# Kernel tuning notes

Measured on AMD Instinct MI355X. Metric: run time of the kernel, lower is better.

Reference implementation:

```python
import jax, jax.numpy as jnp
import numpy as np

H = 128          # hidden/context/decoder dim
HEADS = 4
HEAD_DIM = H // HEADS
MAX_LENGTH = 64
VOCAB = 3


def _lstm_step(h, c, x, Wih, Whh, b):
    # PyTorch gate order: i, f, g, o
    gates = x @ Wih.T + h @ Whh.T + b
    i, f, g, o = jnp.split(gates, 4, axis=-1)
    c = jax.nn.sigmoid(f) * c + jax.nn.sigmoid(i) * jnp.tanh(g)
    h = jax.nn.sigmoid(o) * jnp.tanh(c)
    return h, c


def _run_lstm(x, Wih, Whh, b):
    # x: (T, B, D) -> (T, B, H); zero initial state (PyTorch default)
    B = x.shape[1]
    Hh = Whh.shape[1]
    init = (jnp.zeros((B, Hh), x.dtype), jnp.zeros((B, Hh), x.dtype))
    def step(carry, xt):
        h, c = carry
        h, c = _lstm_step(h, c, xt, Wih, Whh, b)
        return (h, c), h
    _, ys = jax.lax.scan(step, init, x)
    return ys


def setup_inputs() -> dict:
    key = jax.random.key(0)
    T, B, D = 512, 64, 1024
    ks = jax.random.split(key, 20)
    def p(k, shape, s=0.05):
        return jax.random.normal(k, shape, dtype=jnp.float32) * s
    return {
        "cnn_output": p(ks[0], (T, B, D), 1.0),
        # encoder LSTM (2 layers); biases fused (b_ih + b_hh)
        "enc_Wih0": p(ks[1], (4 * H, D)),
        "enc_Whh0": p(ks[2], (4 * H, H)),
        "enc_b0": p(ks[3], (4 * H,)),
        "enc_Wih1": p(ks[4], (4 * H, H)),
        "enc_Whh1": p(ks[5], (4 * H, H)),
        "enc_b1": p(ks[6], (4 * H,)),
        # MultiheadAttention(embed_dim=128, num_heads=4)
        "attn_in_w": p(ks[7], (3 * H, H)),
        "attn_in_b": p(ks[8], (3 * H,)),
        "attn_out_w": p(ks[9], (H, H)),
        "attn_out_b": p(ks[10], (H,)),
        # decoder LSTM (2 layers), input dim 256
        "dec_Wih0": p(ks[11], (4 * H, 2 * H)),
        "dec_Whh0": p(ks[12], (4 * H, H)),
        "dec_b0": p(ks[13], (4 * H,)),
        "dec_Wih1": p(ks[14], (4 * H, H)),
        "dec_Whh1": p(ks[15], (4 * H, H)),
        "dec_b1": p(ks[16], (4 * H,)),
        # output projection
        "lin_w": p(ks[17], (VOCAB, H)),
        "lin_b": p(ks[18], (VOCAB,)),
    }


def reference(cnn_output, enc_Wih0, enc_Whh0, enc_b0, enc_Wih1, enc_Whh1, enc_b1,
              attn_in_w, attn_in_b, attn_out_w, attn_out_b,
              dec_Wih0, dec_Whh0, dec_b0, dec_Wih1, dec_Whh1, dec_b1,
              lin_w, lin_b):
    T, B, _ = cnn_output.shape
    # ---- encoder: 2-layer LSTM over T ----
    enc = _run_lstm(cnn_output, enc_Wih0, enc_Whh0, enc_b0)
    enc = _run_lstm(enc, enc_Wih1, enc_Whh1, enc_b1)          # (T, B, H)

    # ---- precompute attention keys/values (encoding is fixed) ----
    Wq, Wk, Wv = jnp.split(attn_in_w, 3, axis=0)
    bq, bk, bv = jnp.split(attn_in_b, 3, axis=0)
    K = (enc @ Wk.T + bk).reshape(T, B, HEADS, HEAD_DIM)      # (T,B,h,d)
    V = (enc @ Wv.T + bv).reshape(T, B, HEADS, HEAD_DIM)
    scale = 1.0 / np.sqrt(HEAD_DIM)

    # ---- 64-step attention + 2-layer LSTM decode loop ----
    out0 = jnp.zeros((B, H), cnn_output.dtype)
    h0 = jnp.zeros((2, B, H), cnn_output.dtype)
    c0 = jnp.zeros((2, B, H), cnn_output.dtype)

    def step(carry, _):
        out, h, c = carry
        q = ((out @ Wq.T + bq) * scale).reshape(B, HEADS, HEAD_DIM)
        scores = jnp.einsum("bhd,tbhd->bht", q, K)            # (B,h,T)
        attn = jax.nn.softmax(scores, axis=-1)
        ctx = jnp.einsum("bht,tbhd->bhd", attn, V).reshape(B, H)
        ctx = ctx @ attn_out_w.T + attn_out_b
        x = jnp.concatenate([out, ctx], axis=-1)              # (B, 2H)
        nh0, nc0 = _lstm_step(h[0], c[0], x, dec_Wih0, dec_Whh0, dec_b0)
        nh1, nc1 = _lstm_step(h[1], c[1], nh0, dec_Wih1, dec_Whh1, dec_b1)
        new_out = jax.nn.relu(nh1)
        y = new_out @ lin_w.T + lin_b                          # (B, vocab)
        return (new_out, jnp.stack([nh0, nh1]), jnp.stack([nc0, nc1])), y

    _, ys = jax.lax.scan(step, (out0, h0, c0), None, length=MAX_LENGTH)
    return ys                                                  # (64, B, vocab)
```

## Files before the change

### kernel.cpp

```cpp
#include <hip/hip_runtime.h>
#include <math.h>

#define T_LEN 512
#define BATCH 64
#define HID 128
#define G4 512

#define OFF_WQ2   0
#define OFF_WXO   16384
#define OFF_WXC   81920
#define OFF_WHH0b 147456
#define OFF_WIH1b 212992
#define OFF_WHH1b 278528
#define W2_TOTAL  344064

typedef __attribute__((ext_vector_type(8))) short short8b;
typedef __attribute__((ext_vector_type(4))) float f32x4;

__device__ __forceinline__ float sigf(float x) { return 1.0f / (1.0f + __expf(-x)); }
__device__ __forceinline__ float tanhfast(float x) {
    float e = __expf(2.f * x);
    return 1.f - 2.f / (e + 1.f);
}

__device__ __forceinline__ unsigned short f2bf(float x) {
    unsigned u = __float_as_uint(x);
    unsigned r = (u + 0x7fffu + ((u >> 16) & 1u)) >> 16;
    return (unsigned short)r;
}
__device__ __forceinline__ float bf2f(unsigned short u) {
    return __uint_as_float((unsigned)u << 16);
}

__device__ __forceinline__ void cvt8(uint4 u, float f[8]) {
    f[0] = __uint_as_float(u.x << 16); f[1] = __uint_as_float(u.x & 0xffff0000u);
    f[2] = __uint_as_float(u.y << 16); f[3] = __uint_as_float(u.y & 0xffff0000u);
    f[4] = __uint_as_float(u.z << 16); f[5] = __uint_as_float(u.z & 0xffff0000u);
    f[6] = __uint_as_float(u.w << 16); f[7] = __uint_as_float(u.w & 0xffff0000u);
}

#define KEEP4(Vv) asm volatile("" : "+v"((Vv).x), "+v"((Vv).y), "+v"((Vv).z), "+v"((Vv).w))

__device__ __forceinline__ void cstore(float* p, float v) {
    __hip_atomic_store(p, v, __ATOMIC_RELAXED, __HIP_MEMORY_SCOPE_AGENT);
}
__device__ __forceinline__ float cload(float* p) {
    return __hip_atomic_load(p, __ATOMIC_RELAXED, __HIP_MEMORY_SCOPE_AGENT);
}

__global__ __launch_bounds__(256) void pack_bf(
    const float* __restrict__ src, unsigned short* __restrict__ dst, long n8)
{
    long i = (long)blockIdx.x * 256 + threadIdx.x;
    long stride = (long)gridDim.x * 256;
    for (; i < n8; i += stride) {
        const float* s = src + i * 8;
        float4 a = *(const float4*)s;
        float4 b = *(const float4*)(s + 4);
        uint4 o;
        o.x = (unsigned)f2bf(a.x) | ((unsigned)f2bf(a.y) << 16);
        o.y = (unsigned)f2bf(a.z) | ((unsigned)f2bf(a.w) << 16);
        o.z = (unsigned)f2bf(b.x) | ((unsigned)f2bf(b.y) << 16);
        o.w = (unsigned)f2bf(b.z) | ((unsigned)f2bf(b.w) << 16);
        *(uint4*)(dst + i * 8) = o;
    }
}

__global__ __launch_bounds__(256) void gemm_mfma_bf16(
    const unsigned short* __restrict__ A, const unsigned short* __restrict__ B,
    const float* __restrict__ bias, unsigned short* __restrict__ C,
    int M, int N, int K)
{
    __shared__ __align__(16) unsigned char As[128 * 128];
    __shared__ __align__(16) unsigned char Bs[128 * 128];
    const int tid = threadIdx.x;
    const int lane = tid & 63, wave = tid >> 6;
    const int wr = wave >> 1, wc = wave & 1;
    const int m0 = blockIdx.y * 128, n0 = blockIdx.x * 128;
    f32x4 acc[4][4] = {};
    const int lr = lane & 15, g = lane >> 4;

    for (int k0 = 0; k0 < K; k0 += 64) {
        __syncthreads();
        #pragma unroll
        for (int i = 0; i < 4; ++i) {
            int c = tid + i * 256;
            int row = c >> 3, cb = (c & 7) * 16;
            int swz = cb ^ ((row & 7) << 4);
            uint4 va = *(const uint4*)(A + (size_t)(m0 + row) * K + k0 + (c & 7) * 8);
            *(uint4*)(As + row * 128 + swz) = va;
            uint4 vb = *(const uint4*)(B + (size_t)(n0 + row) * K + k0 + (c & 7) * 8);
            *(uint4*)(Bs + row * 128 + swz) = vb;
        }
        __syncthreads();
        #pragma unroll
        for (int kh = 0; kh < 2; ++kh) {
            const int cb = kh * 64 + g * 16;
            short8b af[4], bfr[4];
            #pragma unroll
            for (int m = 0; m < 4; ++m) {
                int row = wr * 64 + m * 16 + lr;
                af[m] = *(const short8b*)(As + row * 128 + (cb ^ ((row & 7) << 4)));
            }
            #pragma unroll
            for (int n = 0; n < 4; ++n) {
                int row = wc * 64 + n * 16 + lr;
                bfr[n] = *(const short8b*)(Bs + row * 128 + (cb ^ ((row & 7) << 4)));
            }
            #pragma unroll
            for (int m = 0; m < 4; ++m)
                #pragma unroll
                for (int n = 0; n < 4; ++n)
                    acc[m][n] = __builtin_amdgcn_mfma_f32_16x16x32_bf16(
                        af[m], bfr[n], acc[m][n], 0, 0, 0);
        }
    }
    #pragma unroll
    for (int n = 0; n < 4; ++n) {
        int col = n0 + wc * 64 + n * 16 + lr;
        float bv = bias[col];
        #pragma unroll
        for (int m = 0; m < 4; ++m) {
            #pragma unroll
            for (int j = 0; j < 4; ++j) {
                int row = m0 + wr * 64 + m * 16 + g * 4 + j;
                C[(size_t)row * N + col] = f2bf(acc[m][n][j] + bv);
            }
        }
    }
}

__global__ __launch_bounds__(1024) void lstm_rec3(
    const unsigned short* __restrict__ X,
    const float* __restrict__ Whh,
    unsigned short* __restrict__ HoutB)
{
    const int b = blockIdx.x;
    const int tid = threadIdx.x;
    const int r = tid >> 1, half = tid & 1;
    __shared__ __align__(16) float h_s[HID];
    __shared__ float gate_s[G4];
    float4 w4[16];
    {
        const float4* wr4 = (const float4*)(Whh + (size_t)r * HID + half * 64);
        #pragma unroll
        for (int i = 0; i < 16; ++i) w4[i] = wr4[i];
    }
    float c = 0.f;
    if (tid < HID) h_s[tid] = 0.f;
    __syncthreads();
    float xc0 = 0.f, xc1 = 0.f, xc2 = 0.f, xc3 = 0.f;
    if (half == 0) {
        xc0 = bf2f(X[(size_t)(0 * BATCH + b) * G4 + r]);
        xc1 = bf2f(X[(size_t)(1 * BATCH + b) * G4 + r]);
        xc2 = bf2f(X[(size_t)(2 * BATCH + b) * G4 + r]);
        xc3 = bf2f(X[(size_t)(3 * BATCH + b) * G4 + r]);
    }
    for (int tc = 0; tc < T_LEN; tc += 4) {
        float xn0 = 0.f, xn1 = 0.f, xn2 = 0.f, xn3 = 0.f;
        if (half == 0 && tc + 4 < T_LEN) {
            xn0 = bf2f(X[(size_t)((tc + 4) * BATCH + b) * G4 + r]);
            xn1 = bf2f(X[(size_t)((tc + 5) * BATCH + b) * G4 + r]);
            xn2 = bf2f(X[(size_t)((tc + 6) * BATCH + b) * G4 + r]);
            xn3 = bf2f(X[(size_t)((tc + 7) * BATCH + b) * G4 + r]);
        }
        #pragma unroll
        for (int i = 0; i < 4; ++i) {
            const int t = tc + i;
            const float xv = (i == 0) ? xc0 : (i == 1) ? xc1 : (i == 2) ? xc2 : xc3;
            float a0 = 0.f, a1 = 0.f, a2 = 0.f, a3 = 0.f;
            const float4* h4 = (const float4*)(h_s + half * 64);
            #pragma unroll
            for (int k = 0; k < 16; ++k) {
                float4 hv = h4[k];
                a0 = fmaf(w4[k].x, hv.x, a0);
                a1 = fmaf(w4[k].y, hv.y, a1);
                a2 = fmaf(w4[k].z, hv.z, a2);
                a3 = fmaf(w4[k].w, hv.w, a3);
            }
            float tot = (a0 + a1) + (a2 + a3);
            tot += __shfl_xor(tot, 1);
            if (half == 0) gate_s[r] = tot + xv;
            __syncthreads();
            if (tid < HID) {
                float gi = gate_s[tid], gf = gate_s[HID+tid], gg = gate_s[2*HID+tid], go = gate_s[3*HID+tid];
                c = sigf(gf) * c + sigf(gi) * tanhfast(gg);
                float h = sigf(go) * tanhfast(c);
                h_s[tid] = h;
                HoutB[(size_t)(t * BATCH + b) * HID + tid] = f2bf(h);
            }
            __syncthreads();
        }
        xc0 = xn0; xc1 = xn1; xc2 = xn2; xc3 = xn3;
    }
}

__global__ __launch_bounds__(256) void kv_pack_bf(
    const unsigned short* __restrict__ KVbf, unsigned short* __restrict__ Kb,
    unsigned short* __restrict__ Vt)
{
    const int b = blockIdx.x & 63, tc = blockIdx.x >> 6;
    const int t0 = tc * 128;
    __shared__ unsigned short tile[128][130];
    const int half = threadIdx.x >> 7;
    const int d = threadIdx.x & 127;
    for (int tt = 0; tt < 128; tt += 2) {
        int trow = tt + half;
        int t = t0 + trow;
        const unsigned short* src = KVbf + ((size_t)t * BATCH + b) * 256;
        Kb[((size_t)b * T_LEN + t) * HID + d] = src[d];
        tile[trow][d] = src[128 + d];
    }
    __syncthreads();
    for (int dd = 0; dd < 128; dd += 2) {
        int drow = dd + half;
        int ts = threadIdx.x & 127;
        Vt[((size_t)b * HID + drow) * T_LEN + t0 + ts] = tile[ts][drow];
    }
}

__global__ __launch_bounds__(256) void pack2(
    const float* __restrict__ attn_in_w,
    const float* __restrict__ dWih0, const float* __restrict__ dWhh0,
    const float* __restrict__ dWih1, const float* __restrict__ dWhh1,
    unsigned short* __restrict__ Wb2)
{
    int i = blockIdx.x * 256 + threadIdx.x;
    if (i >= W2_TOTAL) return;
    if (i >= OFF_WXC && i < OFF_WHH0b) return;
    float v;
    if (i < OFF_WXO) v = attn_in_w[i];
    else if (i < OFF_WXC) {
        int j = i - OFF_WXO; v = dWih0[(size_t)(j >> 7) * 256 + (j & 127)];
    }
    else if (i < OFF_WIH1b) v = dWhh0[i - OFF_WHH0b];
    else if (i < OFF_WHH1b) v = dWih1[i - OFF_WIH1b];
    else                    v = dWhh1[i - OFF_WHH1b];
    Wb2[i] = f2bf(v);
}

__global__ __launch_bounds__(256) void fuse_wxc(
    const float* __restrict__ dWih0, const float* __restrict__ ow,
    unsigned short* __restrict__ Wb2)
{
    __shared__ float ow_s[128 * 128];
    for (int i = threadIdx.x; i < 16384; i += 256) ow_s[i] = ow[i];
    __syncthreads();
    const int r = blockIdx.x * 2 + (threadIdx.x >> 7);
    const int c = threadIdx.x & 127;
    const float* wr = dWih0 + (size_t)r * 256 + 128;
    float acc = 0.f;
    #pragma unroll 8
    for (int j = 0; j < 128; ++j) acc = fmaf(wr[j], ow_s[j * 128 + c], acc);
    Wb2[OFF_WXC + r * 128 + c] = f2bf(acc);
}

__global__ __launch_bounds__(128) void fuse_b0(
    const float* __restrict__ dWih0, const float* __restrict__ ob,
    const float* __restrict__ db0, float* __restrict__ b0p)
{
    int r = blockIdx.x * 128 + threadIdx.x;
    const float* wr = dWih0 + (size_t)r * 256 + 128;
    float acc = db0[r];
    #pragma unroll 8
    for (int j = 0; j < 128; ++j) acc = fmaf(wr[j], ob[j], acc);
    b0p[r] = acc;
}

__global__ __launch_bounds__(512, 2) void decoder7c(
    const unsigned short* __restrict__ Kb, const unsigned short* __restrict__ Vt,
    const unsigned short* __restrict__ Wb2, const float* __restrict__ b0p,
    const float* __restrict__ attn_b, const float* __restrict__ b1,
    const float* __restrict__ lw, const float* __restrict__ lb,
    int* __restrict__ flags, float* __restrict__ exh0, float* __restrict__ exh1,
    float* __restrict__ Y)
{
    extern __shared__ __align__(16) char dyn[];
    char* Kl = dyn;
    const int wid = blockIdx.x;
    const int b = wid & 63;
    const int half64 = wid >> 6;
    const int dbase = half64 * 64;
    const int pbase = 64 - dbase;
    const int tid = threadIdx.x;
    int* myflag = flags + wid * 16;
    int* pflag  = flags + (wid ^ 64) * 16;
    float* exh0b = exh0 + b * 256;
    float* exh1b = exh1 + b * 256;

    __shared__ __align__(16) float x_s[384];
    __shared__ __align__(16) float x1_s[256];
    __shared__ __align__(16) float q_s[HID];
    __shared__ __align__(16) float sc[4 * T_LEN];
    __shared__ float red[512];
    __shared__ __align__(16) float ctxp[4][HID];
    __shared__ float g_s[256];
    __shared__ float hden[4];

    {
        const unsigned short* Ksrc = Kb + (size_t)b * T_LEN * HID;
        for (int c = tid; c < T_LEN * HID / 8; c += 512) {
            int t = c >> 4, k16 = c & 15;
            uint4 v = *(const uint4*)(Ksrc + c * 8);
            *(uint4*)(Kl + t * 256 + ((k16 * 16) ^ ((t & 15) << 4))) = v;
        }
    }
    const int lr = tid >> 1, halfk = tid & 1;
    const int r0 = (lr >> 6) * 128 + dbase + (lr & 63);
    uint4 W0[24], W1[16], WQ[4];
    #pragma unroll
    for (int i = 0; i < 24; ++i) {
        int ge = halfk * 192 + i * 8;
        const unsigned short* src =
            (ge < 128) ? Wb2 + OFF_WXO   + (size_t)r0 * HID + ge
          : (ge < 256) ? Wb2 + OFF_WXC   + (size_t)r0 * HID + (ge - 128)
                       : Wb2 + OFF_WHH0b + (size_t)r0 * HID + (ge - 256);
        W0[i] = *(const uint4*)src;
    }
    #pragma unroll
    for (int i = 0; i < 16; ++i) {
        int ge = halfk * 128 + i * 8;
        const unsigned short* src =
            (ge < 128) ? Wb2 + OFF_WIH1b + (size_t)r0 * HID + ge
                       : Wb2 + OFF_WHH1b + (size_t)r0 * HID + (ge - 128);
        W1[i] = *(const uint4*)src;
    }
    const int qrow = tid >> 2, qpart = tid & 3;
    #pragma unroll
    for (int i = 0; i < 4; ++i)
        WQ[i] = *(const uint4*)(Wb2 + OFF_WQ2 + (size_t)qrow * HID + qpart * 32 + i * 8);
    #pragma unroll
    for (int i = 0; i < 24; ++i) KEEP4(W0[i]);
    #pragma unroll
    for (int i = 0; i < 16; ++i) KEEP4(W1[i]);
    #pragma unroll
    for (int i = 0; i < 4; ++i) KEEP4(WQ[i]);

    const float b0r = b0p[r0];
    const float b1r = b1[r0];
    const float bqv = attn_b[qrow];
    float c0 = 0.f, c1 = 0.f;
    if (tid < 384) x_s[tid] = 0.f;
    if (tid < 256) x1_s[tid] = 0.f;
    __syncthreads();
    const float scale = 0.17677669529663687f;
    const int g = tid >> 7, l = tid & 127;

    for (int step = 0; step < 64; ++step) {
        #pragma unroll
        for (int i = 0; i < 24; ++i) KEEP4(W0[i]);
        #pragma unroll
        for (int i = 0; i < 16; ++i) KEEP4(W1[i]);
        #pragma unroll
        for (int i = 0; i < 4; ++i) KEEP4(WQ[i]);
        const int par = step & 1;
        if (step > 0) {
            if (tid == 0)
                while (__hip_atomic_load(pflag, __ATOMIC_RELAXED, __HIP_MEMORY_SCOPE_AGENT) < 2*step + 1)
                    __builtin_amdgcn_s_sleep(1);
            asm volatile("" ::: "memory");
            __syncthreads();
            if (tid < 64) {
                float hp = cload(&exh1b[((step - 1) & 1) * 128 + pbase + tid]);
                x1_s[128 + pbase + tid] = hp;
                x_s[pbase + tid] = fmaxf(hp, 0.f);
            }
            __syncthreads();
        }
        if (step > 0 && half64 == 0 && tid < 24) {
            const int row = tid >> 3, part = tid & 7;
            const float* wr = lw + row * HID + part * 16;
            const float* os = x_s + part * 16;
            float acc = 0.f;
            #pragma unroll
            for (int k = 0; k < 16; ++k) acc = fmaf(wr[k], os[k], acc);
            acc += __shfl_xor(acc, 1);
            acc += __shfl_xor(acc, 2);
            acc += __shfl_xor(acc, 4);
            if (part == 0) Y[((size_t)(step - 1) * BATCH + b) * 3 + row] = acc + lb[row];
        }
        {
            float acc = 0.f;
            const float* os = x_s + qpart * 32;
            #pragma unroll
            for (int i = 0; i < 4; ++i) {
                float f[8]; cvt8(WQ[i], f);
                const float* o8 = os + i * 8;
                acc += f[0]*o8[0]+f[1]*o8[1]+f[2]*o8[2]+f[3]*o8[3]
                     + f[4]*o8[4]+f[5]*o8[5]+f[6]*o8[6]+f[7]*o8[7];
            }
            acc += __shfl_xor(acc, 1);
            acc += __shfl_xor(acc, 2);
            if (qpart == 0) q_s[qrow] = (acc + bqv) * scale;
        }
        __syncthreads();
        {
            const int t = tid;
            float acc[4] = {0.f, 0.f, 0.f, 0.f};
            #pragma unroll
            for (int k16 = 0; k16 < 16; ++k16) {
                uint4 u = *(const uint4*)(Kl + t * 256 + ((k16 * 16) ^ ((t & 15) << 4)));
                float f[8]; cvt8(u, f);
                float4 q0 = *(const float4*)(q_s + k16 * 8);
                float4 q1 = *(const float4*)(q_s + k16 * 8 + 4);
                acc[k16 >> 2] += f[0]*q0.x + f[1]*q0.y + f[2]*q0.z + f[3]*q0.w
                               + f[4]*q1.x + f[5]*q1.y + f[6]*q1.z + f[7]*q1.w;
            }
            #pragma unroll
            for (int h = 0; h < 4; ++h) sc[h * T_LEN + t] = __expf(acc[h]);
        }
        __syncthreads();
        {
            float s4 = 0.f;
            #pragma unroll
            for (int i = 0; i < 4; ++i) s4 += sc[g * T_LEN + l + 128 * i];
            red[tid] = s4;
        }
        __syncthreads();
        if (l < 64) {
            float s2 = red[g*128 + l] + red[g*128 + l + 64];
            #pragma unroll
            for (int s = 32; s > 0; s >>= 1) s2 += __shfl_xor(s2, s, 64);
            if (l == 0) hden[g] = s2;
        }
        __syncthreads();
        {
            const int d = tid & 127, ch = tid >> 7;
            const unsigned short* vr = Vt + ((size_t)b * HID + d) * T_LEN + ch * 128;
            const float* scr = sc + (d >> 5) * T_LEN + ch * 128;
            float acc = 0.f;
            #pragma unroll
            for (int k = 0; k < 128; k += 8) {
                float f[8]; cvt8(*(const uint4*)(vr + k), f);
                #pragma unroll
                for (int j = 0; j < 8; ++j) acc = fmaf(f[j], scr[k + j], acc);
            }
            ctxp[ch][d] = acc;
        }
        __syncthreads();
        if (tid < HID)
            x_s[HID + tid] = (ctxp[0][tid] + ctxp[1][tid] + ctxp[2][tid] + ctxp[3][tid]) / hden[tid >> 5];
        __syncthreads();
        {
            float acc = 0.f;
            #pragma unroll
            for (int i = 0; i < 24; ++i) {
                float f[8]; cvt8(W0[i], f);
                const float* xp = x_s + halfk * 192 + i * 8;
                acc += f[0]*xp[0]+f[1]*xp[1]+f[2]*xp[2]+f[3]*xp[3]
                     + f[4]*xp[4]+f[5]*xp[5]+f[6]*xp[6]+f[7]*xp[7];
            }
            acc += __shfl_xor(acc, 1);
            if (halfk == 0) g_s[lr] = acc + b0r;
        }
        __syncthreads();
        if (tid < 64) {
            float gi = g_s[tid], gf = g_s[64+tid], gg = g_s[128+tid], go = g_s[192+tid];
            c0 = sigf(gf) * c0 + sigf(gi) * tanhf(gg);
            float h = sigf(go) * tanhf(c0);
            x_s[256 + dbase + tid] = h;
            x1_s[dbase + tid] = h;
            cstore(&exh0b[par * 128 + dbase + tid], h);
        }
        __syncthreads();
        if (tid == 0) {
            asm volatile("s_waitcnt vmcnt(0)" ::: "memory");
            __hip_atomic_store(myflag, 2*step + 2, __ATOMIC_RELEASE, __HIP_MEMORY_SCOPE_AGENT);
        }
        if (tid == 0)
            while (__hip_atomic_load(pflag, __ATOMIC_ACQUIRE, __HIP_MEMORY_SCOPE_AGENT) < 2*step + 2)
                __builtin_amdgcn_s_sleep(1);
        asm volatile("" ::: "memory");
        __syncthreads();
        if (tid < 64) {
            float hp = cload(&exh0b[par * 128 + pbase + tid]);
            x_s[256 + pbase + tid] = hp;
            x1_s[pbase + tid] = hp;
        }
        __syncthreads();
        {
            float acc = 0.f;
            #pragma unroll
            for (int i = 0; i < 16; ++i) {
                float f[8]; cvt8(W1[i], f);
                const float* xp = x1_s + halfk * 128 + i * 8;
                acc += f[0]*xp[0]+f[1]*xp[1]+f[2]*xp[2]+f[3]*xp[3]
                     + f[4]*xp[4]+f[5]*xp[5]+f[6]*xp[6]+f[7]*xp[7];
            }
            acc += __shfl_xor(acc, 1);
            if (halfk == 0) g_s[lr] = acc + b1r;
        }
        __syncthreads();
        if (tid < 64) {
            float gi = g_s[tid], gf = g_s[64+tid], gg = g_s[128+tid], go = g_s[192+tid];
            c1 = sigf(gf) * c1 + sigf(gi) * tanhf(gg);
            float h = sigf(go) * tanhf(c1);
            x1_s[128 + dbase + tid] = h;
            x_s[dbase + tid] = fmaxf(h, 0.f);
            cstore(&exh1b[par * 128 + dbase + tid], h);
        }
        __syncthreads();
        if (tid == 0) {
            asm volatile("s_waitcnt vmcnt(0)" ::: "memory");
            __hip_atomic_store(myflag, 2*step + 3, __ATOMIC_RELEASE, __HIP_MEMORY_SCOPE_AGENT);
        }
        __syncthreads();
    }
    if (tid == 0)
        while (__hip_atomic_load(pflag, __ATOMIC_ACQUIRE, __HIP_MEMORY_SCOPE_AGENT) < 129)
            __builtin_amdgcn_s_sleep(1);
    asm volatile("" ::: "memory");
    __syncthreads();
    if (tid < 64)
        x_s[pbase + tid] = fmaxf(cload(&exh1b[128 + pbase + tid]), 0.f);
    __syncthreads();
    if (half64 == 0 && tid < 24) {
        const int row = tid >> 3, part = tid & 7;
        const float* wr = lw + row * HID + part * 16;
        const float* os = x_s + part * 16;
        float acc = 0.f;
        #pragma unroll
        for (int k = 0; k < 16; ++k) acc = fmaf(wr[k], os[k], acc);
        acc += __shfl_xor(acc, 1);
        acc += __shfl_xor(acc, 2);
        acc += __shfl_xor(acc, 4);
        if (part == 0) Y[((size_t)63 * BATCH + b) * 3 + row] = acc + lb[row];
    }
}

extern "C" void kernel_launch(void* const* d_in, const int* in_sizes, int n_in,
                              void* d_out, int out_size, void* d_ws, size_t ws_size,
                              hipStream_t stream) {
    const float* cnn        = (const float*)d_in[0];
    const float* eWih0      = (const float*)d_in[1];
    const float* eWhh0      = (const float*)d_in[2];
    const float* eb0        = (const float*)d_in[3];
    const float* eWih1      = (const float*)d_in[4];
    const float* eWhh1      = (const float*)d_in[5];
    const float* eb1        = (const float*)d_in[6];
    const float* attn_in_w  = (const float*)d_in[7];
    const float* attn_in_b  = (const float*)d_in[8];
    const float* attn_out_w = (const float*)d_in[9];
    const float* attn_out_b = (const float*)d_in[10];
    const float* dWih0      = (const float*)d_in[11];
    const float* dWhh0      = (const float*)d_in[12];
    const float* db0        = (const float*)d_in[13];
    const float* dWih1      = (const float*)d_in[14];
    const float* dWhh1      = (const float*)d_in[15];
    const float* db1        = (const float*)d_in[16];
    const float* lin_w      = (const float*)d_in[17];
    const float* lin_b      = (const float*)d_in[18];
    float* Y  = (float*)d_out;

    const int M = T_LEN * BATCH;

    char* wsb = (char*)d_ws;
    unsigned short* Xbf   = (unsigned short*)(wsb);
    unsigned short* Hbf   = (unsigned short*)(wsb + ((size_t)32 << 20));
    unsigned short* wih0b = (unsigned short*)(wsb + ((size_t)40 << 20));
    unsigned short* wih1b = (unsigned short*)(wsb + ((size_t)41 << 20));
    unsigned short* wkvb  = (unsigned short*)(wsb + ((size_t)41 << 20) + (512 << 10));
    unsigned short* Wb2   = (unsigned short*)(wsb + ((size_t)42 << 20));
    float* b0p   = (float*)(wsb + ((size_t)43 << 20));
    int*   flags = (int*)((char*)b0p + 4096);
    float* exh0  = (float*)((char*)flags + 16384);
    float* exh1  = exh0 + 64 * 256;
    unsigned short* cnn_bf = (unsigned short*)(wsb + ((size_t)44 << 20));
    unsigned short* KVbf   = cnn_bf;
    unsigned short* Kb     = (unsigned short*)(wsb + ((size_t)60 << 20));
    unsigned short* Vt     = (unsigned short*)(wsb + ((size_t)68 << 20));

    (void)hipFuncSetAttribute((const void*)decoder7c,
                              hipFuncAttributeMaxDynamicSharedMemorySize, 131072);

    pack_bf<<<2048, 256, 0, stream>>>(cnn, cnn_bf, (long)M * 1024 / 8);
    pack_bf<<<256, 256, 0, stream>>>(eWih0, wih0b, (long)512 * 1024 / 8);
    pack_bf<<<32, 256, 0, stream>>>(eWih1, wih1b, (long)512 * 128 / 8);
    pack_bf<<<16, 256, 0, stream>>>(attn_in_w + 128 * 128, wkvb, (long)256 * 128 / 8);
    gemm_mfma_bf16<<<dim3(4, M/128), 256, 0, stream>>>(cnn_bf, wih0b, eb0, Xbf, M, 512, 1024);
    (void)hipMemsetAsync(flags, 0, 16384 + 2 * 64 * 256 * 4, stream);
    pack2<<<(W2_TOTAL + 255) / 256, 256, 0, stream>>>(attn_in_w, dWih0, dWhh0, dWih1, dWhh1, Wb2);
    fuse_wxc<<<256, 256, 0, stream>>>(dWih0, attn_out_w, Wb2);
    fuse_b0<<<4, 128, 0, stream>>>(dWih0, attn_out_b, db0, b0p);
    lstm_rec3<<<BATCH, 1024, 0, stream>>>(Xbf, eWhh0, Hbf);
    gemm_mfma_bf16<<<dim3(4, M/128), 256, 0, stream>>>(Hbf, wih1b, eb1, Xbf, M, 512, 128);
    lstm_rec3<<<BATCH, 1024, 0, stream>>>(Xbf, eWhh1, Hbf);
    gemm_mfma_bf16<<<dim3(2, M/128), 256, 0, stream>>>(Hbf, wkvb, attn_in_b + 128, KVbf, M, 256, 128);
    kv_pack_bf<<<256, 256, 0, stream>>>(KVbf, Kb, Vt);
    decoder7c<<<128, 512, 131072, stream>>>(Kb, Vt, Wb2, b0p,
                                            attn_in_b, db1, lin_w, lin_b,
                                            flags, exh0, exh1, Y);
}
```

Before: 2.419 ms.

## Fuse two encoder LSTM layers into one wavefront-pipelined kernel with flags

Replaces the two sequential encoder LSTM launches and the layer-1 input GEMM with one kernel of 128 blocks. Blocks 0-63 run layer 0 and publish each h_t to global memory with a release flag. Blocks 64-127 spin on that flag and compute layer 1 with the input projection done inline from bf16 weights held in registers. This lets the two recurrences overlap in time instead of running back to back. The cost is cross-block spin synchronisation, per-step global round trips, and a requirement that all 128 blocks be co-resident, otherwise the kernel deadlocks.

Result: slower. 3.592 ms (+48.5%).

```diff
diff --git a/kernel.cpp b/kernel.cpp
--- a/kernel.cpp
+++ b/kernel.cpp
@@ -130,57 +130,130 @@
     }
 }
 
-__global__ __launch_bounds__(1024) void lstm_rec3(
+__global__ __launch_bounds__(1024, 1) void lstm_fused(
     const unsigned short* __restrict__ X,
-    const float* __restrict__ Whh,
+    const float* __restrict__ Whh0,
+    const unsigned short* __restrict__ Wih1b,
+    const unsigned short* __restrict__ Whh1b,
+    const float* __restrict__ b1v,
+    float* __restrict__ h0x,
+    int* __restrict__ lflags,
     unsigned short* __restrict__ HoutB)
 {
-    const int b = blockIdx.x;
+    const int wid = blockIdx.x;
+    const int b = wid & 63;
     const int tid = threadIdx.x;
     const int r = tid >> 1, half = tid & 1;
+    int* flag = lflags + b * 16;
     __shared__ __align__(16) float h_s[HID];
+    __shared__ __align__(16) float x0_s[HID];
     __shared__ float gate_s[G4];
-    float4 w4[16];
-    {
-        const float4* wr4 = (const float4*)(Whh + (size_t)r * HID + half * 64);
-        #pragma unroll
-        for (int i = 0; i < 16; ++i) w4[i] = wr4[i];
-    }
-    float c = 0.f;
-    if (tid < HID) h_s[tid] = 0.f;
-    __syncthreads();
-    float xc0 = 0.f, xc1 = 0.f, xc2 = 0.f, xc3 = 0.f;
-    if (half == 0) {
-        xc0 = bf2f(X[(size_t)(0 * BATCH + b) * G4 + r]);
-        xc1 = bf2f(X[(size_t)(1 * BATCH + b) * G4 + r]);
-        xc2 = bf2f(X[(size_t)(2 * BATCH + b) * G4 + r]);
-        xc3 = bf2f(X[(size_t)(3 * BATCH + b) * G4 + r]);
-    }
-    for (int tc = 0; tc < T_LEN; tc += 4) {
-        float xn0 = 0.f, xn1 = 0.f, xn2 = 0.f, xn3 = 0.f;
-        if (half == 0 && tc + 4 < T_LEN) {
-            xn0 = bf2f(X[(size_t)((tc + 4) * BATCH + b) * G4 + r]);
-            xn1 = bf2f(X[(size_t)((tc + 5) * BATCH + b) * G4 + r]);
-            xn2 = bf2f(X[(size_t)((tc + 6) * BATCH + b) * G4 + r]);
-            xn3 = bf2f(X[(size_t)((tc + 7) * BATCH + b) * G4 + r]);
-        }
-        #pragma unroll
-        for (int i = 0; i < 4; ++i) {
-            const int t = tc + i;
-            const float xv = (i == 0) ? xc0 : (i == 1) ? xc1 : (i == 2) ? xc2 : xc3;
-            float a0 = 0.f, a1 = 0.f, a2 = 0.f, a3 = 0.f;
-            const float4* h4 = (const float4*)(h_s + half * 64);
-            #pragma unroll
-            for (int k = 0; k < 16; ++k) {
-                float4 hv = h4[k];
-                a0 = fmaf(w4[k].x, hv.x, a0);
-                a1 = fmaf(w4[k].y, hv.y, a1);
-                a2 = fmaf(w4[k].z, hv.z, a2);
-                a3 = fmaf(w4[k].w, hv.w, a3);
-            }
-            float tot = (a0 + a1) + (a2 + a3);
-            tot += __shfl_xor(tot, 1);
-            if (half == 0) gate_s[r] = tot + xv;
+
+    if (wid < 64) {
+        float4 w4[16];
+        {
+            const float4* wr4 = (const float4*)(Whh0 + (size_t)r * HID + half * 64);
+            #pragma unroll
+            for (int i = 0; i < 16; ++i) w4[i] = wr4[i];
+        }
+        float c = 0.f;
+        if (tid < HID) h_s[tid] = 0.f;
+        __syncthreads();
+        float xc0 = 0.f, xc1 = 0.f, xc2 = 0.f, xc3 = 0.f;
+        if (half == 0) {
+            xc0 = bf2f(X[(size_t)(0 * BATCH + b) * G4 + r]);
+            xc1 = bf2f(X[(size_t)(1 * BATCH + b) * G4 + r]);
+            xc2 = bf2f(X[(size_t)(2 * BATCH + b) * G4 + r]);
+            xc3 = bf2f(X[(size_t)(3 * BATCH + b) * G4 + r]);
+        }
+        for (int tc = 0; tc < T_LEN; tc += 4) {
+            float xn0 = 0.f, xn1 = 0.f, xn2 = 0.f, xn3 = 0.f;
+            if (half == 0 && tc + 4 < T_LEN) {
+                xn0 = bf2f(X[(size_t)((tc + 4) * BATCH + b) * G4 + r]);
+                xn1 = bf2f(X[(size_t)((tc + 5) * BATCH + b) * G4 + r]);
+                xn2 = bf2f(X[(size_t)((tc + 6) * BATCH + b) * G4 + r]);
+                xn3 = bf2f(X[(size_t)((tc + 7) * BATCH + b) * G4 + r]);
+            }
+            #pragma unroll
+            for (int i = 0; i < 4; ++i) {
+                const int t = tc + i;
+                const float xv = (i == 0) ? xc0 : (i == 1) ? xc1 : (i == 2) ? xc2 : xc3;
+                float a0 = 0.f, a1 = 0.f, a2 = 0.f, a3 = 0.f;
+                const float4* h4 = (const float4*)(h_s + half * 64);
+                #pragma unroll
+                for (int k = 0; k < 16; ++k) {
+                    float4 hv = h4[k];
+                    a0 = fmaf(w4[k].x, hv.x, a0);
+                    a1 = fmaf(w4[k].y, hv.y, a1);
+                    a2 = fmaf(w4[k].z, hv.z, a2);
+                    a3 = fmaf(w4[k].w, hv.w, a3);
+                }
+                float tot = (a0 + a1) + (a2 + a3);
+                tot += __shfl_xor(tot, 1);
+                if (half == 0) gate_s[r] = tot + xv;
+                __syncthreads();
+                if (tid < HID) {
+                    float gi = gate_s[tid], gf = gate_s[HID+tid], gg = gate_s[2*HID+tid], go = gate_s[3*HID+tid];
+                    c = sigf(gf) * c + sigf(gi) * tanhfast(gg);
+                    h_s[tid] = sigf(go) * tanhfast(c);
+                }
+                __syncthreads();
+                if (tid < 64) {
+                    float* row = h0x + ((size_t)t * BATCH + b) * HID;
+                    cstore(row + tid, h_s[tid]);
+                    cstore(row + tid + 64, h_s[tid + 64]);
+                }
+                if (tid == 0) {
+                    asm volatile("s_waitcnt vmcnt(0)" ::: "memory");
+                    __hip_atomic_store(flag, t + 1, __ATOMIC_RELEASE, __HIP_MEMORY_SCOPE_AGENT);
+                }
+            }
+            xc0 = xn0; xc1 = xn1; xc2 = xn2; xc3 = xn3;
+        }
+    } else {
+        uint4 wi[8], wh[8];
+        {
+            const unsigned short* ps = Wih1b + (size_t)r * HID + half * 64;
+            const unsigned short* qs = Whh1b + (size_t)r * HID + half * 64;
+            #pragma unroll
+            for (int i = 0; i < 8; ++i) wi[i] = *(const uint4*)(ps + i * 8);
+            #pragma unroll
+            for (int i = 0; i < 8; ++i) wh[i] = *(const uint4*)(qs + i * 8);
+        }
+        const float b1r = b1v[r];
+        float c = 0.f;
+        if (tid < HID) h_s[tid] = 0.f;
+        __syncthreads();
+        for (int t = 0; t < T_LEN; ++t) {
+            if (tid == 0)
+                while (__hip_atomic_load(flag, __ATOMIC_ACQUIRE, __HIP_MEMORY_SCOPE_AGENT) < t + 1)
+                    __builtin_amdgcn_s_sleep(1);
+            asm volatile("" ::: "memory");
+            __syncthreads();
+            if (tid < HID)
+                x0_s[tid] = cload(h0x + ((size_t)t * BATCH + b) * HID + tid);
+            __syncthreads();
+            float acc = 0.f;
+            {
+                const float* xp = x0_s + half * 64;
+                const float* hp = h_s + half * 64;
+                #pragma unroll
+                for (int i = 0; i < 8; ++i) {
+                    float f[8]; cvt8(wi[i], f);
+                    const float* x8 = xp + i * 8;
+                    acc += f[0]*x8[0]+f[1]*x8[1]+f[2]*x8[2]+f[3]*x8[3]
+                         + f[4]*x8[4]+f[5]*x8[5]+f[6]*x8[6]+f[7]*x8[7];
+                }
+                #pragma unroll
+                for (int i = 0; i < 8; ++i) {
+                    float f[8]; cvt8(wh[i], f);
+                    const float* h8 = hp + i * 8;
+                    acc += f[0]*h8[0]+f[1]*h8[1]+f[2]*h8[2]+f[3]*h8[3]
+                         + f[4]*h8[4]+f[5]*h8[5]+f[6]*h8[6]+f[7]*h8[7];
+                }
+            }
+            acc += __shfl_xor(acc, 1);
+            if (half == 0) gate_s[r] = acc + b1r;
             __syncthreads();
             if (tid < HID) {
                 float gi = gate_s[tid], gf = gate_s[HID+tid], gg = gate_s[2*HID+tid], go = gate_s[3*HID+tid];
@@ -191,7 +264,6 @@
             }
             __syncthreads();
         }
-        xc0 = xn0; xc1 = xn1; xc2 = xn2; xc3 = xn3;
     }
 }
 
@@ -559,16 +631,19 @@
     unsigned short* Hbf   = (unsigned short*)(wsb + ((size_t)32 << 20));
     unsigned short* wih0b = (unsigned short*)(wsb + ((size_t)40 << 20));
     unsigned short* wih1b = (unsigned short*)(wsb + ((size_t)41 << 20));
+    unsigned short* whh1b = (unsigned short*)(wsb + ((size_t)41 << 20) + (128 << 10));
     unsigned short* wkvb  = (unsigned short*)(wsb + ((size_t)41 << 20) + (512 << 10));
     unsigned short* Wb2   = (unsigned short*)(wsb + ((size_t)42 << 20));
     float* b0p   = (float*)(wsb + ((size_t)43 << 20));
     int*   flags = (int*)((char*)b0p + 4096);
     float* exh0  = (float*)((char*)flags + 16384);
     float* exh1  = exh0 + 64 * 256;
+    int*   lstmflags = (int*)(wsb + ((size_t)43 << 20) + (512 << 10));
     unsigned short* cnn_bf = (unsigned short*)(wsb + ((size_t)44 << 20));
     unsigned short* KVbf   = cnn_bf;
     unsigned short* Kb     = (unsigned short*)(wsb + ((size_t)60 << 20));
     unsigned short* Vt     = (unsigned short*)(wsb + ((size_t)68 << 20));
+    float* h0x = (float*)(wsb + ((size_t)76 << 20));
 
     (void)hipFuncSetAttribute((const void*)decoder7c,
                               hipFuncAttributeMaxDynamicSharedMemorySize, 131072);
@@ -576,15 +651,16 @@
     pack_bf<<<2048, 256, 0, stream>>>(cnn, cnn_bf, (long)M * 1024 / 8);
     pack_bf<<<256, 256, 0, stream>>>(eWih0, wih0b, (long)512 * 1024 / 8);
     pack_bf<<<32, 256, 0, stream>>>(eWih1, wih1b, (long)512 * 128 / 8);
+    pack_bf<<<32, 256, 0, stream>>>(eWhh1, whh1b, (long)512 * 128 / 8);
     pack_bf<<<16, 256, 0, stream>>>(attn_in_w + 128 * 128, wkvb, (long)256 * 128 / 8);
     gemm_mfma_bf16<<<dim3(4, M/128), 256, 0, stream>>>(cnn_bf, wih0b, eb0, Xbf, M, 512, 1024);
     (void)hipMemsetAsync(flags, 0, 16384 + 2 * 64 * 256 * 4, stream);
+    (void)hipMemsetAsync(lstmflags, 0, 64 * 16 * 4, stream);
     pack2<<<(W2_TOTAL + 255) / 256, 256, 0, stream>>>(attn_in_w, dWih0, dWhh0, dWih1, dWhh1, Wb2);
     fuse_wxc<<<256, 256, 0, stream>>>(dWih0, attn_out_w, Wb2);
     fuse_b0<<<4, 128, 0, stream>>>(dWih0, attn_out_b, db0, b0p);
-    lstm_rec3<<<BATCH, 1024, 0, stream>>>(Xbf, eWhh0, Hbf);
-    gemm_mfma_bf16<<<dim3(4, M/128), 256, 0, stream>>>(Hbf, wih1b, eb1, Xbf, M, 512, 128);
-    lstm_rec3<<<BATCH, 1024, 0, stream>>>(Xbf, eWhh1, Hbf);
+    lstm_fused<<<128, 1024, 0, stream>>>(Xbf, eWhh0, wih1b, whh1b, eb1,
+                                         h0x, lstmflags, Hbf);
     gemm_mfma_bf16<<<dim3(2, M/128), 256, 0, stream>>>(Hbf, wkvb, attn_in_b + 128, KVbf, M, 256, 128);
     kv_pack_bf<<<256, 256, 0, stream>>>(KVbf, Kb, Vt);
     decoder7c<<<128, 512, 131072, stream>>>(Kb, Vt, Wb2, b0p,
```
